# Kernel tuning notes

Hardware: AMD Instinct MI355X
Metric: run time of the kernel (lower is better)

## Reference

```python
import jax, jax.numpy as jnp
import numpy as np

H = 128
S = 65  # 64 board cells + 1 appended bias token


def _attn(y, wk, wq, wv):
    # y: [B, H, S]
    k = jnp.einsum('ij,bjs->bis', wk, y)
    q = jnp.einsum('ij,bjs->bis', wq, y)
    v = jnp.einsum('ij,bjs->bis', wv, y)
    kq = jnp.einsum('bis,bit->bst', k, q)          # k.T @ q -> [B, S, S]
    sm = jax.nn.softmax(kq, axis=-1)               # softmax over dim=1 of [S,S]
    return jnp.einsum('bst,bit->bsi', sm, v)       # sm @ v.T -> [B, S, H]


def setup_inputs() -> dict:
    key = jax.random.key(0)
    ks = jax.random.split(key, 17)
    B = 8192
    d = dict(
        inputs=jax.random.normal(ks[0], (1, B, 64), jnp.float32),
        embeding=jax.random.normal(ks[1], (H, S), jnp.float32),
        w_k11=jax.random.normal(ks[2], (H, H), jnp.float32),
        w_q11=jax.random.normal(ks[3], (H, H), jnp.float32),
        w_v11=jax.random.normal(ks[4], (H, H), jnp.float32),
        w_k12=jax.random.normal(ks[5], (H, H), jnp.float32),
        w_q12=jax.random.normal(ks[6], (H, H), jnp.float32),
        w_v12=jax.random.normal(ks[7], (H, H), jnp.float32),
        linear1=jax.random.normal(ks[8], (2 * H, H), jnp.float32),
        w_k21=jax.random.normal(ks[9], (H, H), jnp.float32),
        w_q21=jax.random.normal(ks[10], (H, H), jnp.float32),
        w_v21=jax.random.normal(ks[11], (H, H), jnp.float32),
        w_k22=jax.random.normal(ks[12], (H, H), jnp.float32),
        w_q22=jax.random.normal(ks[13], (H, H), jnp.float32),
        w_v22=jax.random.normal(ks[14], (H, H), jnp.float32),
        linear2=jax.random.normal(ks[15], (2 * H, H), jnp.float32),
        linear3=jax.random.normal(ks[16], (H, H // 2), jnp.float32),
        linear4=jax.random.normal(jax.random.fold_in(key, 99), (H // 2, 1), jnp.float32),
    )
    return d


def reference(inputs, embeding, w_k11, w_q11, w_v11, w_k12, w_q12, w_v12, linear1,
              w_k21, w_q21, w_v21, w_k22, w_q22, w_v22, linear2, linear3, linear4):
    xb = inputs[0]                                   # [B, 64]
    B = xb.shape[0]
    x = jnp.concatenate([xb, jnp.ones((B, 1), xb.dtype)], axis=1)  # [B, 65]
    y = embeding[None, :, :] * x[:, None, :]         # [B, H, S]

    att11 = _attn(y, w_k11, w_q11, w_v11)            # [B, S, H]
    att12 = _attn(y, w_k12, w_q12, w_v12)
    y = jnp.tanh(jnp.concatenate([att11, att12], axis=-1) @ linear1)  # [B, S, H]
    y = jnp.swapaxes(y, 1, 2)                        # [B, H, S]

    att21 = _attn(y, w_k21, w_q21, w_v21)
    att22 = _attn(y, w_k22, w_q22, w_v22)
    y = jnp.tanh(jnp.concatenate([att21, att22], axis=-1) @ linear2)  # [B, S, H]
    y = y[:, 64, :]                                  # take bias token -> [B, H]
    y = jnp.tanh(y @ linear3)                        # [B, H//2]
    score = y @ linear4                              # [B, 1]
    return score[:, 0][None, :]                      # [1, B]
```

## Files before the change

### kernel.cpp

```cpp
#include <hip/hip_runtime.h>
#include <math.h>


#define YQ(s, q) ((s) * 128 + 4 * ((q) ^ ((s) & 7)))
#define KA_STR 68
#define QA_STR 72
#define QA_BASE 4420

__global__
__attribute__((amdgpu_flat_work_group_size(512, 512)))
__attribute__((amdgpu_waves_per_eu(4, 8)))
void literal_kernel(const float* __restrict__ in0,
                    const float* __restrict__ emb,
                    const float* __restrict__ wk11, const float* __restrict__ wq11,
                    const float* __restrict__ wv11,
                    const float* __restrict__ wk12, const float* __restrict__ wq12,
                    const float* __restrict__ wv12,
                    const float* __restrict__ l1,
                    const float* __restrict__ wk21, const float* __restrict__ wq21,
                    const float* __restrict__ wv21,
                    const float* __restrict__ wk22, const float* __restrict__ wq22,
                    const float* __restrict__ wv22,
                    const float* __restrict__ l2,
                    const float* __restrict__ L3, const float* __restrict__ L4,
                    float* __restrict__ out)
{
    __shared__ __align__(16) float vsh[8320];
    __shared__ __align__(16) float R1[9028];
    __shared__ __align__(16) float k64sh[128];
    __shared__ __align__(16) float q64sh[128];
    __shared__ float kq64sh[68];
    __shared__ __align__(16) float smr[68];
    __shared__ __align__(16) float attr[128];
    __shared__ float y4sh[128];

    const int tid  = threadIdx.x;
    const int lane = tid & 63;
    const int wu   = __builtin_amdgcn_readfirstlane(tid >> 6);
    const long b   = blockIdx.x;
    const float xr = in0[b * 64 + lane];

    float* kA = R1;
    float* qA = R1 + QA_BASE;

    const int h4 = (tid & 31) * 4;
    const int sb = tid >> 5;
    float4 acc1[4];
    #pragma unroll
    for (int si = 0; si < 4; ++si) acc1[si] = make_float4(0.f, 0.f, 0.f, 0.f);

    for (int a = 0; a < 2; ++a) {
        const float* wk = a ? wk12 : wk11;
        const float* wq = a ? wq12 : wq11;
        const float* wv = a ? wv12 : wv11;

        float kqa[8];
        #pragma unroll
        for (int m = 0; m < 8; ++m) kqa[m] = 0.f;
        float kq64acc = 0.f, kqr64acc = 0.f, corner = 0.f;

        for (int p = 0; p < 2; ++p) {
            const int ip0 = p * 64 + wu * 8;
            float aK[8], aQ[8], aV[8];
            #pragma unroll
            for (int r = 0; r < 8; ++r) { aK[r] = aQ[r] = aV[r] = 0.f; }
            float acc64 = 0.f;
            {
                const int ch = lane >> 3;
                const float* Wc = (ch == 0) ? wk : ((ch == 1) ? wq : wv);
                const float* wcrow = Wc + (ip0 + (lane & 7)) * 128;
                for (int jq = 0; jq < 32; ++jq) {
                    const float* erow = emb + (jq * 4) * 65;
                    float yv[4];
                    #pragma unroll
                    for (int u = 0; u < 4; ++u) yv[u] = erow[u * 65 + lane] * xr;
                    #pragma unroll
                    for (int r = 0; r < 8; ++r) {
                        const float* wkr = wk + (ip0 + r) * 128 + jq * 4;
                        const float* wqr = wq + (ip0 + r) * 128 + jq * 4;
                        const float* wvr = wv + (ip0 + r) * 128 + jq * 4;
                        #pragma unroll
                        for (int u = 0; u < 4; ++u) {
                            aK[r] = fmaf(wkr[u], yv[u], aK[r]);
                            aQ[r] = fmaf(wqr[u], yv[u], aQ[r]);
                            aV[r] = fmaf(wvr[u], yv[u], aV[r]);
                        }
                    }
                    if (lane < 24) {
                        float4 c0 = *(const float4*)&wcrow[jq * 4];
                        acc64 = fmaf(c0.x, erow[0 * 65 + 64], acc64);
                        acc64 = fmaf(c0.y, erow[1 * 65 + 64], acc64);
                        acc64 = fmaf(c0.z, erow[2 * 65 + 64], acc64);
                        acc64 = fmaf(c0.w, erow[3 * 65 + 64], acc64);
                    }
                }
                *(float4*)&kA[lane * KA_STR + wu * 8]     = make_float4(aK[0], aK[1], aK[2], aK[3]);
                *(float4*)&kA[lane * KA_STR + wu * 8 + 4] = make_float4(aK[4], aK[5], aK[6], aK[7]);
                *(float4*)&qA[lane * QA_STR + wu * 8]     = make_float4(aQ[0], aQ[1], aQ[2], aQ[3]);
                *(float4*)&qA[lane * QA_STR + wu * 8 + 4] = make_float4(aQ[4], aQ[5], aQ[6], aQ[7]);
                #pragma unroll
                for (int r = 0; r < 8; ++r) vsh[(ip0 + r) * 65 + lane] = aV[r];
                if (lane < 8)            k64sh[ip0 + lane] = acc64;
                else if (lane < 16)      q64sh[ip0 + (lane & 7)] = acc64;
                else if (lane < 24)      vsh[(ip0 + (lane & 7)) * 65 + 64] = acc64;
            }
            __syncthreads();

            for (int iq = 0; iq < 16; ++iq) {
                float4 qq = *(const float4*)&qA[lane * QA_STR + iq * 4];
                #pragma unroll
                for (int m = 0; m < 8; ++m) {
                    float4 kk = *(const float4*)&kA[(wu + 8 * m) * KA_STR + iq * 4];
                    kqa[m] = fmaf(kk.x, qq.x, kqa[m]);
                    kqa[m] = fmaf(kk.y, qq.y, kqa[m]);
                    kqa[m] = fmaf(kk.z, qq.z, kqa[m]);
                    kqa[m] = fmaf(kk.w, qq.w, kqa[m]);
                }
                if (wu == 0) {
                    float4 kc = *(const float4*)&k64sh[p * 64 + iq * 4];
                    float4 qc = *(const float4*)&q64sh[p * 64 + iq * 4];
                    kqr64acc = fmaf(kc.x, qq.x, kqr64acc);
                    kqr64acc = fmaf(kc.y, qq.y, kqr64acc);
                    kqr64acc = fmaf(kc.z, qq.z, kqr64acc);
                    kqr64acc = fmaf(kc.w, qq.w, kqr64acc);
                    float4 ks = *(const float4*)&kA[lane * KA_STR + iq * 4];
                    kq64acc = fmaf(ks.x, qc.x, kq64acc);
                    kq64acc = fmaf(ks.y, qc.y, kq64acc);
                    kq64acc = fmaf(ks.z, qc.z, kq64acc);
                    kq64acc = fmaf(ks.w, qc.w, kq64acc);
                    if (lane == 0) {
                        corner = fmaf(kc.x, qc.x, corner);
                        corner = fmaf(kc.y, qc.y, corner);
                        corner = fmaf(kc.z, qc.z, corner);
                        corner = fmaf(kc.w, qc.w, corner);
                    }
                }
            }
            if (p == 1 && wu == 0) {
                kq64sh[lane] = kq64acc;
                if (lane == 0) kq64sh[64] = corner;
            }
            __syncthreads();
        }

        float smv[9], sm64v[9];
        #pragma unroll
        for (int m = 0; m < 9; ++m) { smv[m] = 0.f; sm64v[m] = 0.f; }
        #pragma unroll
        for (int m = 0; m < 9; ++m) {
            if (m < 8 || wu == 0) {
                int s = (m == 8) ? 64 : (wu + 8 * m);
                float lg   = (m == 8) ? kqr64acc : kqa[m];
                float l64v = (lane == 0) ? kq64sh[s] : -3.0e38f;
                float mm = fmaxf(lg, l64v);
                #pragma unroll
                for (int off = 32; off >= 1; off >>= 1) mm = fmaxf(mm, __shfl_xor(mm, off));
                float e   = expf(lg - mm);
                float e64 = (lane == 0) ? expf(l64v - mm) : 0.f;
                float zs = e + e64;
                #pragma unroll
                for (int off = 32; off >= 1; off >>= 1) zs += __shfl_xor(zs, off);
                float inv = 1.0f / zs;
                smv[m] = e * inv;
                sm64v[m] = e64 * inv;
            }
        }
        {
            float aa0[9], aa1[9];
            #pragma unroll
            for (int m = 0; m < 9; ++m) { aa0[m] = 0.f; aa1[m] = 0.f; }
            const float* vr0 = &vsh[lane * 65];
            const float* vr1 = &vsh[(lane + 64) * 65];
            for (int t = 0; t < 64; ++t) {
                float v0 = vr0[t], v1 = vr1[t];
                #pragma unroll
                for (int m = 0; m < 9; ++m) {
                    if (m < 8 || wu == 0) {
                        float smt = __shfl(smv[m], t);
                        aa0[m] = fmaf(smt, v0, aa0[m]);
                        aa1[m] = fmaf(smt, v1, aa1[m]);
                    }
                }
            }
            float v0e = vr0[64], v1e = vr1[64];
            #pragma unroll
            for (int m = 0; m < 9; ++m) {
                if (m < 8 || wu == 0) {
                    float smt = __shfl(sm64v[m], 0);
                    aa0[m] = fmaf(smt, v0e, aa0[m]);
                    aa1[m] = fmaf(smt, v1e, aa1[m]);
                    int s = (m == 8) ? 64 : (wu + 8 * m);
                    R1[s * 128 + lane]      = aa0[m];
                    R1[s * 128 + lane + 64] = aa1[m];
                }
            }
        }
        __syncthreads();

        if (a == 0 && tid < 128) attr[tid] = R1[64 * 128 + tid];

        {
            const float* l1a = l1 + a * 16384;
            for (int i0b = 0; i0b < 128; i0b += 4) {
                float4 av0 = *(const float4*)&R1[(sb +  0) * 128 + i0b];
                float4 av1 = *(const float4*)&R1[(sb + 16) * 128 + i0b];
                float4 av2 = *(const float4*)&R1[(sb + 32) * 128 + i0b];
                float4 av3 = *(const float4*)&R1[(sb + 48) * 128 + i0b];
                float a0[4] = { av0.x, av0.y, av0.z, av0.w };
                float a1[4] = { av1.x, av1.y, av1.z, av1.w };
                float a2[4] = { av2.x, av2.y, av2.z, av2.w };
                float a3[4] = { av3.x, av3.y, av3.z, av3.w };
                #pragma unroll
                for (int r = 0; r < 4; ++r) {
                    float4 lv = *(const float4*)&l1a[(i0b + r) * 128 + h4];
                    acc1[0].x = fmaf(a0[r], lv.x, acc1[0].x);
                    acc1[0].y = fmaf(a0[r], lv.y, acc1[0].y);
                    acc1[0].z = fmaf(a0[r], lv.z, acc1[0].z);
                    acc1[0].w = fmaf(a0[r], lv.w, acc1[0].w);
                    acc1[1].x = fmaf(a1[r], lv.x, acc1[1].x);
                    acc1[1].y = fmaf(a1[r], lv.y, acc1[1].y);
                    acc1[1].z = fmaf(a1[r], lv.z, acc1[1].z);
                    acc1[1].w = fmaf(a1[r], lv.w, acc1[1].w);
                    acc1[2].x = fmaf(a2[r], lv.x, acc1[2].x);
                    acc1[2].y = fmaf(a2[r], lv.y, acc1[2].y);
                    acc1[2].z = fmaf(a2[r], lv.z, acc1[2].z);
                    acc1[2].w = fmaf(a2[r], lv.w, acc1[2].w);
                    acc1[3].x = fmaf(a3[r], lv.x, acc1[3].x);
                    acc1[3].y = fmaf(a3[r], lv.y, acc1[3].y);
                    acc1[3].z = fmaf(a3[r], lv.z, acc1[3].z);
                    acc1[3].w = fmaf(a3[r], lv.w, acc1[3].w);
                }
            }
        }
        __syncthreads();
    }

    if (tid < 128) {
        const float* l1a0 = l1;
        const float* l1a1 = l1 + 16384;
        float acc = 0.f;
        for (int i = 0; i < 128; ++i) acc = fmaf(attr[i],        l1a0[i * 128 + tid], acc);
        for (int i = 0; i < 128; ++i) acc = fmaf(R1[64*128 + i], l1a1[i * 128 + tid], acc);
        vsh[YQ(64, tid >> 2) + (tid & 3)] = tanhf(acc);
    }
    #pragma unroll
    for (int si = 0; si < 4; ++si) {
        int s = sb + 16 * si;
        float4 tq;
        tq.x = tanhf(acc1[si].x);
        tq.y = tanhf(acc1[si].y);
        tq.z = tanhf(acc1[si].z);
        tq.w = tanhf(acc1[si].w);
        *(float4*)&vsh[YQ(s, h4 >> 2)] = tq;
    }
    __syncthreads();

    float pre2 = 0.f;
    for (int a2 = 0; a2 < 2; ++a2) {
        const float* wk2 = a2 ? wk22 : wk21;
        const float* wq2 = a2 ? wq22 : wq21;
        const float* wv2 = a2 ? wv22 : wv21;

        float kq2acc = 0.f, corner2 = 0.f;

        for (int p = 0; p < 2; ++p) {
            const int ip0 = p * 64 + wu * 8;
            float aQ[8];
            #pragma unroll
            for (int r = 0; r < 8; ++r) aQ[r] = 0.f;
            float acc64 = 0.f;
            {
                const int ch = lane >> 3;
                const float* Wc = (ch == 0) ? wq2 : wk2;
                const float* wcrow = Wc + (ip0 + (lane & 7)) * 128;
                for (int jq = 0; jq < 32; ++jq) {
                    float4 yq = *(const float4*)&vsh[YQ(lane, jq)];
                    float yv[4] = { yq.x, yq.y, yq.z, yq.w };
                    #pragma unroll
                    for (int r = 0; r < 8; ++r) {
                        const float* wqr = wq2 + (ip0 + r) * 128 + jq * 4;
                        #pragma unroll
                        for (int u = 0; u < 4; ++u)
                            aQ[r] = fmaf(wqr[u], yv[u], aQ[r]);
                    }
                    if (lane < 16) {
                        float4 zq = *(const float4*)&vsh[YQ(64, jq)];
                        float4 c0 = *(const float4*)&wcrow[jq * 4];
                        acc64 = fmaf(c0.x, zq.x, acc64);
                        acc64 = fmaf(c0.y, zq.y, acc64);
                        acc64 = fmaf(c0.z, zq.z, acc64);
                        acc64 = fmaf(c0.w, zq.w, acc64);
                    }
                }
                *(float4*)&qA[lane * QA_STR + wu * 8]     = make_float4(aQ[0], aQ[1], aQ[2], aQ[3]);
                *(float4*)&qA[lane * QA_STR + wu * 8 + 4] = make_float4(aQ[4], aQ[5], aQ[6], aQ[7]);
                if (lane < 8)            q64sh[ip0 + lane] = acc64;
                else if (lane < 16)      k64sh[ip0 + (lane & 7)] = acc64;
            }
            __syncthreads();

            if (wu == 0) {
                for (int iq = 0; iq < 16; ++iq) {
                    float4 qq = *(const float4*)&qA[lane * QA_STR + iq * 4];
                    float4 kk = *(const float4*)&k64sh[p * 64 + iq * 4];
                    kq2acc = fmaf(kk.x, qq.x, kq2acc);
                    kq2acc = fmaf(kk.y, qq.y, kq2acc);
                    kq2acc = fmaf(kk.z, qq.z, kq2acc);
                    kq2acc = fmaf(kk.w, qq.w, kq2acc);
                    if (lane == 0) {
                        float4 qz = *(const float4*)&q64sh[p * 64 + iq * 4];
                        corner2 = fmaf(kk.x, qz.x, corner2);
                        corner2 = fmaf(kk.y, qz.y, corner2);
                        corner2 = fmaf(kk.z, qz.z, corner2);
                        corner2 = fmaf(kk.w, qz.w, corner2);
                    }
                }
            }
            __syncthreads();
        }

        if (wu == 0) {
            float lg   = kq2acc;
            float l64v = (lane == 0) ? corner2 : -3.0e38f;
            float mm = fmaxf(lg, l64v);
            #pragma unroll
            for (int off = 32; off >= 1; off >>= 1) mm = fmaxf(mm, __shfl_xor(mm, off));
            float e   = expf(lg - mm);
            float e64 = (lane == 0) ? expf(l64v - mm) : 0.f;
            float zs = e + e64;
            #pragma unroll
            for (int off = 32; off >= 1; off >>= 1) zs += __shfl_xor(zs, off);
            float inv = 1.0f / zs;
            smr[lane] = e * inv;
            if (lane == 0) smr[64] = e64 * inv;
        }
        __syncthreads();

        if (tid < 128) {
            float uacc = 0.f;
            for (int t = 0; t <= 64; ++t)
                uacc = fmaf(smr[t], vsh[YQ(t, tid >> 2) + (tid & 3)], uacc);
            k64sh[tid] = uacc;
        }
        __syncthreads();

        if (tid < 128) {
            const float* wvrow = wv2 + tid * 128;
            float acc = 0.f;
            for (int h0 = 0; h0 < 128; h0 += 4) {
                float4 wq4 = *(const float4*)&wvrow[h0];
                acc = fmaf(wq4.x, k64sh[h0 + 0], acc);
                acc = fmaf(wq4.y, k64sh[h0 + 1], acc);
                acc = fmaf(wq4.z, k64sh[h0 + 2], acc);
                acc = fmaf(wq4.w, k64sh[h0 + 3], acc);
            }
            attr[tid] = acc;
        }
        __syncthreads();

        {
            const int hh = tid & 127, cc = tid >> 7;
            const float* l2a = l2 + a2 * 16384;
            float pp = 0.f;
            #pragma unroll
            for (int g = 0; g < 8; ++g) {
                int i = cc * 32 + 4 * g;
                float4 av = *(const float4*)&attr[i];
                pp = fmaf(av.x, l2a[(i + 0) * 128 + hh], pp);
                pp = fmaf(av.y, l2a[(i + 1) * 128 + hh], pp);
                pp = fmaf(av.z, l2a[(i + 2) * 128 + hh], pp);
                pp = fmaf(av.w, l2a[(i + 3) * 128 + hh], pp);
            }
            R1[cc * 128 + hh] = pp;
        }
        __syncthreads();
        if (tid < 128) {
            float red = R1[tid];
            #pragma unroll
            for (int c = 1; c < 4; ++c) red += R1[c * 128 + tid];
            pre2 += red;
        }
        __syncthreads();
    }

    if (tid < 128) y4sh[tid] = tanhf(pre2);
    __syncthreads();

    {
        const int oo = tid & 63, cc = tid >> 6;
        float pp = 0.f;
        #pragma unroll
        for (int u = 0; u < 16; ++u) {
            int h = cc * 16 + u;
            pp = fmaf(y4sh[h], L3[h * 64 + oo], pp);
        }
        R1[cc * 64 + oo] = pp;
    }
    __syncthreads();
    if (tid < 64) {
        float t3 = R1[tid];
        #pragma unroll
        for (int c = 1; c < 8; ++c) t3 += R1[c * 64 + tid];
        float y5 = tanhf(t3);
        float sc = y5 * L4[tid];
        #pragma unroll
        for (int off = 32; off >= 1; off >>= 1) sc += __shfl_xor(sc, off);
        if (tid == 0) out[b] = sc;
    }
}

extern "C" void kernel_launch(void* const* d_in, const int* in_sizes, int n_in,
                              void* d_out, int out_size, void* d_ws, size_t ws_size,
                              hipStream_t stream) {
    const float* in0  = (const float*)d_in[0];
    const float* emb  = (const float*)d_in[1];
    const float* wk11 = (const float*)d_in[2];
    const float* wq11 = (const float*)d_in[3];
    const float* wv11 = (const float*)d_in[4];
    const float* wk12 = (const float*)d_in[5];
    const float* wq12 = (const float*)d_in[6];
    const float* wv12 = (const float*)d_in[7];
    const float* l1   = (const float*)d_in[8];
    const float* wk21 = (const float*)d_in[9];
    const float* wq21 = (const float*)d_in[10];
    const float* wv21 = (const float*)d_in[11];
    const float* wk22 = (const float*)d_in[12];
    const float* wq22 = (const float*)d_in[13];
    const float* wv22 = (const float*)d_in[14];
    const float* l2   = (const float*)d_in[15];
    const float* l3   = (const float*)d_in[16];
    const float* l4   = (const float*)d_in[17];
    float* out = (float*)d_out;

    int B = in_sizes[0] / 64;

    literal_kernel<<<B, 512, 0, stream>>>(in0, emb,
                                          wk11, wq11, wv11, wk12, wq12, wv12, l1,
                                          wk21, wq21, wv21, wk22, wq22, wv22, l2,
                                          l3, l4, out);
}
```

Baseline: 5.402 ms.

## Split K/Q and V projections, stage softmax in LDS, remap sm@V across all threads

Result: slower. 12.93 ms (+139.4%).

```diff
diff --git a/kernel.cpp b/kernel.cpp
--- a/kernel.cpp
+++ b/kernel.cpp
@@ -25,7 +25,7 @@
                     const float* __restrict__ L3, const float* __restrict__ L4,
                     float* __restrict__ out)
 {
-    __shared__ __align__(16) float vsh[8320];
+    __shared__ __align__(16) float vsh[128 * 68];
     __shared__ __align__(16) float R1[9028];
     __shared__ __align__(16) float k64sh[128];
     __shared__ __align__(16) float q64sh[128];
@@ -40,8 +40,9 @@
     const long b   = blockIdx.x;
     const float xr = in0[b * 64 + lane];
 
-    float* kA = R1;
-    float* qA = R1 + QA_BASE;
+    float* kA  = R1;
+    float* qA  = R1 + QA_BASE;
+    float* ATT = R1 + QA_BASE;
 
     const int h4 = (tid & 31) * 4;
     const int sb = tid >> 5;
@@ -61,13 +62,13 @@
 
         for (int p = 0; p < 2; ++p) {
             const int ip0 = p * 64 + wu * 8;
-            float aK[8], aQ[8], aV[8];
-            #pragma unroll
-            for (int r = 0; r < 8; ++r) { aK[r] = aQ[r] = aV[r] = 0.f; }
-            float acc64 = 0.f;
+
             {
-                const int ch = lane >> 3;
-                const float* Wc = (ch == 0) ? wk : ((ch == 1) ? wq : wv);
+                float aK[8], aQ[8];
+                #pragma unroll
+                for (int r = 0; r < 8; ++r) { aK[r] = 0.f; aQ[r] = 0.f; }
+                float acc64 = 0.f;
+                const float* Wc = (lane < 8) ? wk : wq;
                 const float* wcrow = Wc + (ip0 + (lane & 7)) * 128;
                 for (int jq = 0; jq < 32; ++jq) {
                     const float* erow = emb + (jq * 4) * 65;
@@ -78,15 +79,13 @@
                     for (int r = 0; r < 8; ++r) {
                         const float* wkr = wk + (ip0 + r) * 128 + jq * 4;
                         const float* wqr = wq + (ip0 + r) * 128 + jq * 4;
-                        const float* wvr = wv + (ip0 + r) * 128 + jq * 4;
                         #pragma unroll
                         for (int u = 0; u < 4; ++u) {
                             aK[r] = fmaf(wkr[u], yv[u], aK[r]);
                             aQ[r] = fmaf(wqr[u], yv[u], aQ[r]);
-                            aV[r] = fmaf(wvr[u], yv[u], aV[r]);
                         }
                     }
-                    if (lane < 24) {
+                    if (lane < 16) {
                         float4 c0 = *(const float4*)&wcrow[jq * 4];
                         acc64 = fmaf(c0.x, erow[0 * 65 + 64], acc64);
                         acc64 = fmaf(c0.y, erow[1 * 65 + 64], acc64);
@@ -98,11 +97,38 @@
                 *(float4*)&kA[lane * KA_STR + wu * 8 + 4] = make_float4(aK[4], aK[5], aK[6], aK[7]);
                 *(float4*)&qA[lane * QA_STR + wu * 8]     = make_float4(aQ[0], aQ[1], aQ[2], aQ[3]);
                 *(float4*)&qA[lane * QA_STR + wu * 8 + 4] = make_float4(aQ[4], aQ[5], aQ[6], aQ[7]);
-                #pragma unroll
-                for (int r = 0; r < 8; ++r) vsh[(ip0 + r) * 65 + lane] = aV[r];
-                if (lane < 8)            k64sh[ip0 + lane] = acc64;
-                else if (lane < 16)      q64sh[ip0 + (lane & 7)] = acc64;
-                else if (lane < 24)      vsh[(ip0 + (lane & 7)) * 65 + 64] = acc64;
+                if (lane < 8)       k64sh[ip0 + lane] = acc64;
+                else if (lane < 16) q64sh[ip0 + (lane & 7)] = acc64;
+            }
+            {
+                float aV[8];
+                #pragma unroll
+                for (int r = 0; r < 8; ++r) aV[r] = 0.f;
+                float acc64 = 0.f;
+                const float* wcrow = wv + (ip0 + (lane & 7)) * 128;
+                for (int jq = 0; jq < 32; ++jq) {
+                    const float* erow = emb + (jq * 4) * 65;
+                    float yv[4];
+                    #pragma unroll
+                    for (int u = 0; u < 4; ++u) yv[u] = erow[u * 65 + lane] * xr;
+                    #pragma unroll
+                    for (int r = 0; r < 8; ++r) {
+                        const float* wvr = wv + (ip0 + r) * 128 + jq * 4;
+                        #pragma unroll
+                        for (int u = 0; u < 4; ++u)
+                            aV[r] = fmaf(wvr[u], yv[u], aV[r]);
+                    }
+                    if (lane >= 16 && lane < 24) {
+                        float4 c0 = *(const float4*)&wcrow[jq * 4];
+                        acc64 = fmaf(c0.x, erow[0 * 65 + 64], acc64);
+                        acc64 = fmaf(c0.y, erow[1 * 65 + 64], acc64);
+                        acc64 = fmaf(c0.z, erow[2 * 65 + 64], acc64);
+                        acc64 = fmaf(c0.w, erow[3 * 65 + 64], acc64);
+                    }
+                }
+                #pragma unroll
+                for (int r = 0; r < 8; ++r) vsh[(ip0 + r) * 68 + lane] = aV[r];
+                if (lane >= 16 && lane < 24) vsh[(ip0 + (lane & 7)) * 68 + 64] = acc64;
             }
             __syncthreads();
 
@@ -143,9 +169,6 @@
             __syncthreads();
         }
 
-        float smv[9], sm64v[9];
-        #pragma unroll
-        for (int m = 0; m < 9; ++m) { smv[m] = 0.f; sm64v[m] = 0.f; }
         #pragma unroll
         for (int m = 0; m < 9; ++m) {
             if (m < 8 || wu == 0) {
@@ -161,51 +184,90 @@
                 #pragma unroll
                 for (int off = 32; off >= 1; off >>= 1) zs += __shfl_xor(zs, off);
                 float inv = 1.0f / zs;
-                smv[m] = e * inv;
-                sm64v[m] = e64 * inv;
-            }
-        }
+                R1[s * 68 + lane] = e * inv;
+                if (lane == 0) R1[s * 68 + 64] = e64 * inv;
+            }
+        }
+        __syncthreads();
+
         {
-            float aa0[9], aa1[9];
-            #pragma unroll
-            for (int m = 0; m < 9; ++m) { aa0[m] = 0.f; aa1[m] = 0.f; }
-            const float* vr0 = &vsh[lane * 65];
-            const float* vr1 = &vsh[(lane + 64) * 65];
-            for (int t = 0; t < 64; ++t) {
-                float v0 = vr0[t], v1 = vr1[t];
+            const int iA = tid & 127;
+            const int sg = tid >> 7;
+            float aa[8];
+            #pragma unroll
+            for (int m = 0; m < 8; ++m) aa[m] = 0.f;
+            const float* vr = &vsh[iA * 68];
+            for (int k = 0; k < 16; ++k) {
+                float4 vq = *(const float4*)&vr[4 * k];
+                #pragma unroll
+                for (int m = 0; m < 8; ++m) {
+                    int s = sg + 4 * m;
+                    float4 sq = *(const float4*)&R1[s * 68 + 4 * k];
+                    aa[m] = fmaf(sq.x, vq.x, aa[m]);
+                    aa[m] = fmaf(sq.y, vq.y, aa[m]);
+                    aa[m] = fmaf(sq.z, vq.z, aa[m]);
+                    aa[m] = fmaf(sq.w, vq.w, aa[m]);
+                }
+            }
+            float v64 = vr[64];
+            #pragma unroll
+            for (int m = 0; m < 8; ++m) {
+                int s = sg + 4 * m;
+                aa[m] = fmaf(R1[s * 68 + 64], v64, aa[m]);
+                ATT[s * 128 + iA] = aa[m];
+            }
+        }
+        __syncthreads();
+
+        {
+            const int iA = tid & 127;
+            const int sg = tid >> 7;
+            float aa[9];
+            #pragma unroll
+            for (int m = 0; m < 9; ++m) aa[m] = 0.f;
+            const float* vr = &vsh[iA * 68];
+            for (int k = 0; k < 16; ++k) {
+                float4 vq = *(const float4*)&vr[4 * k];
                 #pragma unroll
                 for (int m = 0; m < 9; ++m) {
-                    if (m < 8 || wu == 0) {
-                        float smt = __shfl(smv[m], t);
-                        aa0[m] = fmaf(smt, v0, aa0[m]);
-                        aa1[m] = fmaf(smt, v1, aa1[m]);
-                    }
-                }
-            }
-            float v0e = vr0[64], v1e = vr1[64];
+                    if (m < 8 || sg == 0) {
+                        int s = (m == 8) ? 64 : (32 + sg + 4 * m);
+                        float4 sq = *(const float4*)&R1[s * 68 + 4 * k];
+                        aa[m] = fmaf(sq.x, vq.x, aa[m]);
+                        aa[m] = fmaf(sq.y, vq.y, aa[m]);
+                        aa[m] = fmaf(sq.z, vq.z, aa[m]);
+                        aa[m] = fmaf(sq.w, vq.w, aa[m]);
+                    }
+                }
+            }
+            float v64 = vr[64];
             #pragma unroll
             for (int m = 0; m < 9; ++m) {
-                if (m < 8 || wu == 0) {
-                    float smt = __shfl(sm64v[m], 0);
-                    aa0[m] = fmaf(smt, v0e, aa0[m]);
-                    aa1[m] = fmaf(smt, v1e, aa1[m]);
-                    int s = (m == 8) ? 64 : (wu + 8 * m);
-                    R1[s * 128 + lane]      = aa0[m];
-                    R1[s * 128 + lane + 64] = aa1[m];
-                }
-            }
-        }
-        __syncthreads();
-
-        if (a == 0 && tid < 128) attr[tid] = R1[64 * 128 + tid];
+                if (m < 8 || sg == 0) {
+                    int s = (m == 8) ? 64 : (32 + sg + 4 * m);
+                    aa[m] = fmaf(R1[s * 68 + 64], v64, aa[m]);
+                }
+            }
+            __syncthreads();
+            #pragma unroll
+            for (int m = 0; m < 9; ++m) {
+                if (m < 8 || sg == 0) {
+                    int srel = (m == 8) ? 32 : (sg + 4 * m);
+                    R1[srel * 128 + iA] = aa[m];
+                }
+            }
+        }
+        __syncthreads();
+
+        if (a == 0 && tid < 128) attr[tid] = R1[32 * 128 + tid];
 
         {
             const float* l1a = l1 + a * 16384;
             for (int i0b = 0; i0b < 128; i0b += 4) {
-                float4 av0 = *(const float4*)&R1[(sb +  0) * 128 + i0b];
-                float4 av1 = *(const float4*)&R1[(sb + 16) * 128 + i0b];
-                float4 av2 = *(const float4*)&R1[(sb + 32) * 128 + i0b];
-                float4 av3 = *(const float4*)&R1[(sb + 48) * 128 + i0b];
+                float4 av0 = *(const float4*)&ATT[(sb +  0) * 128 + i0b];
+                float4 av1 = *(const float4*)&ATT[(sb + 16) * 128 + i0b];
+                float4 av2 = *(const float4*)&R1[(sb +  0) * 128 + i0b];
+                float4 av3 = *(const float4*)&R1[(sb + 16) * 128 + i0b];
                 float a0[4] = { av0.x, av0.y, av0.z, av0.w };
                 float a1[4] = { av1.x, av1.y, av1.z, av1.w };
                 float a2[4] = { av2.x, av2.y, av2.z, av2.w };
@@ -236,11 +298,9 @@
     }
 
     if (tid < 128) {
-        const float* l1a0 = l1;
-        const float* l1a1 = l1 + 16384;
         float acc = 0.f;
-        for (int i = 0; i < 128; ++i) acc = fmaf(attr[i],        l1a0[i * 128 + tid], acc);
-        for (int i = 0; i < 128; ++i) acc = fmaf(R1[64*128 + i], l1a1[i * 128 + tid], acc);
+        for (int i = 0; i < 128; ++i) acc = fmaf(attr[i],      l1[i * 128 + tid], acc);
+        for (int i = 0; i < 128; ++i) acc = fmaf(R1[4096 + i], l1[16384 + i * 128 + tid], acc);
         vsh[YQ(64, tid >> 2) + (tid & 3)] = tanhf(acc);
     }
     #pragma unroll
@@ -270,8 +330,7 @@
             for (int r = 0; r < 8; ++r) aQ[r] = 0.f;
             float acc64 = 0.f;
             {
-                const int ch = lane >> 3;
-                const float* Wc = (ch == 0) ? wq2 : wk2;
+                const float* Wc = (lane < 8) ? wq2 : wk2;
                 const float* wcrow = Wc + (ip0 + (lane & 7)) * 128;
                 for (int jq = 0; jq < 32; ++jq) {
                     float4 yq = *(const float4*)&vsh[YQ(lane, jq)];
@@ -294,8 +353,8 @@
                 }
                 *(float4*)&qA[lane * QA_STR + wu * 8]     = make_float4(aQ[0], aQ[1], aQ[2], aQ[3]);
                 *(float4*)&qA[lane * QA_STR + wu * 8 + 4] = make_float4(aQ[4], aQ[5], aQ[6], aQ[7]);
-                if (lane < 8)            q64sh[ip0 + lane] = acc64;
-                else if (lane < 16)      k64sh[ip0 + (lane & 7)] = acc64;
+                if (lane < 8)       q64sh[ip0 + lane] = acc64;
+                else if (lane < 16) k64sh[ip0 + (lane & 7)] = acc64;
             }
             __syncthreads();
 
```
